# Kernel tuning notes

Hardware: AMD Instinct MI355X
Metric: run time of the kernel (lower is better)

The kernel has to match this reference:

```python
import jax, jax.numpy as jnp
import numpy as np

N_NODES = 100000
N_EDGES = 600000
D = 128
L = 4
BN_EPS = 1e-5


def setup_inputs() -> dict:
    key = jax.random.key(0)
    ks = jax.random.split(key, 12)
    x = jax.random.normal(ks[0], (N_NODES, D), dtype=jnp.float32)
    edge_index = jax.random.randint(ks[1], (2, N_EDGES), 0, N_NODES, dtype=jnp.int64)
    edge_attr = jax.random.uniform(ks[2], (N_EDGES, 1), dtype=jnp.float32)
    s = 0.05
    return {
        'x': x,
        'edge_index': edge_index,
        'edge_attr': edge_attr,
        'We': jax.random.normal(ks[3], (L, 1, D), dtype=jnp.float32) * s,   # GINE edge projection Linear(1, D)
        'be': jnp.zeros((L, D), dtype=jnp.float32),
        'eps': jnp.zeros((L,), dtype=jnp.float32),                          # train_eps=True, init 0
        'W1': jax.random.normal(ks[4], (L, D, D), dtype=jnp.float32) * s,
        'b1': jnp.zeros((L, D), dtype=jnp.float32),
        'gamma': jnp.ones((L, D), dtype=jnp.float32),
        'beta': jnp.zeros((L, D), dtype=jnp.float32),
        'W2': jax.random.normal(ks[5], (L, D, D), dtype=jnp.float32) * s,
        'b2': jnp.zeros((L, D), dtype=jnp.float32),
    }


def _gine_layer(h, src, dst, edge_attr, We, be, eps, W1, b1, gamma, beta, W2, b2):
    n = h.shape[0]
    e = edge_attr @ We + be                       # [E, D] edge embedding
    m = jax.nn.relu(h[src] + e)                   # gather + add + relu (messages)
    agg = jax.ops.segment_sum(m, dst, num_segments=n)  # scatter-add to destination nodes
    z = (1.0 + eps) * h + agg
    # MLP: Linear -> BatchNorm1d (training stats) -> ReLU -> Linear
    z = z @ W1 + b1
    mu = jnp.mean(z, axis=0)
    var = jnp.var(z, axis=0)                      # biased var, as in torch BN training
    z = (z - mu) * jax.lax.rsqrt(var + BN_EPS) * gamma + beta
    z = jax.nn.relu(z)
    return z @ W2 + b2


def reference(x, edge_index, edge_attr, We, be, eps, W1, b1, gamma, beta, W2, b2):
    src, dst = edge_index[0], edge_index[1]
    h = x
    for l in range(L):
        z = _gine_layer(h, src, dst, edge_attr, We[l], be[l], eps[l],
                        W1[l], b1[l], gamma[l], beta[l], W2[l], b2[l])
        r = jax.nn.relu(z)
        h = r if l == 0 else h + r
    return h
```

## Files before the change

kernel.cpp:

```cpp
#include <hip/hip_runtime.h>

#define NN 100000
#define NE 600000
#define DD 128
#define NL 4
#define GB 512
#define BKS 9
#define NBK ((NN + 511) >> 9)
#define CH 4096

typedef __attribute__((ext_vector_type(8))) short short8;
typedef __attribute__((ext_vector_type(4))) float float4v;
typedef __attribute__((ext_vector_type(2))) float f2;

__device__ inline unsigned short f2bf(float f) {
  union { float f; unsigned u; } v; v.f = f;
  unsigned r = v.u + 0x7fff + ((v.u >> 16) & 1);
  return (unsigned short)(r >> 16);
}
__device__ inline float bf2f(unsigned short u) {
  union { unsigned u; float f; } v; v.u = ((unsigned)u) << 16;
  return v.f;
}
__device__ inline f2 bfpair(unsigned u) {
  f2 r;
  r.x = __uint_as_float(u << 16);
  r.y = __uint_as_float(u & 0xffff0000u);
  return r;
}

__global__ void k_prep(const float* __restrict__ W1, const float* __restrict__ W2,
                       unsigned short* __restrict__ WT, int* __restrict__ counts,
                       float* __restrict__ stats4) {
  int i = blockIdx.x * 256 + threadIdx.x;
  if (i < NN) counts[i] = 0;
  if (i < NL * 256) stats4[i] = 0.f;
  if (i >= 8 * 16384) return;
  int m = i >> 14;
  int el = i & 16383;
  int k = el >> 7;
  int n = el & 127;
  const float* src = (m < 4) ? (W1 + (size_t)m * 16384) : (W2 + (size_t)(m - 4) * 16384);
  WT[(size_t)m * 16384 + n * 128 + k] = f2bf(src[k * 128 + n]);
}

__global__ void k_h2b(const float* __restrict__ src, unsigned short* __restrict__ dst,
                      const int* __restrict__ ei, int* __restrict__ counts) {
  int i = blockIdx.x * 256 + threadIdx.x;
  if (i < NE) atomicAdd(&counts[ei[NE + i]], 1);
  if (i >= NN * DD / 4) return;
  float4 v = ((const float4*)src)[i];
  ushort4 o;
  o.x = f2bf(v.x); o.y = f2bf(v.y); o.z = f2bf(v.z); o.w = f2bf(v.w);
  ((ushort4*)dst)[i] = o;
}

#define ST 256
#define SC 2
#define SB ((NN + ST * SC - 1) / (ST * SC))

__global__ void k_scan_part(const int* __restrict__ counts, int* __restrict__ row_ptr,
                            int* __restrict__ bsums) {
  __shared__ int s[ST];
  int b = blockIdx.x, t = threadIdx.x;
  int base = b * (ST * SC) + t * SC;
  int v0 = (base < NN) ? counts[base] : 0;
  int v1 = (base + 1 < NN) ? counts[base + 1] : 0;
  int tsum = v0 + v1;
  s[t] = tsum;
  __syncthreads();
  for (int d = 1; d < ST; d <<= 1) {
    int x = (t >= d) ? s[t - d] : 0;
    __syncthreads();
    s[t] += x;
    __syncthreads();
  }
  int excl = s[t] - tsum;
  if (base < NN) row_ptr[base] = excl;
  if (base + 1 < NN) row_ptr[base + 1] = excl + v0;
  if (t == ST - 1) bsums[b] = s[t];
}

__global__ void k_scan_bsum(const int* __restrict__ bsums, int* __restrict__ boffs,
                            int* __restrict__ row_ptr) {
  __shared__ int s[ST];
  int t = threadIdx.x;
  int v = (t < SB) ? bsums[t] : 0;
  s[t] = v;
  __syncthreads();
  for (int d = 1; d < ST; d <<= 1) {
    int x = (t >= d) ? s[t - d] : 0;
    __syncthreads();
    s[t] += x;
    __syncthreads();
  }
  if (t < SB) boffs[t] = s[t] - v;
  if (t == ST - 1) row_ptr[NN] = s[t];
}

__global__ void k_scan_add(const int* __restrict__ boffs, int* __restrict__ row_ptr,
                           int* __restrict__ scur) {
  int b = blockIdx.x, t = threadIdx.x;
  int base = b * (ST * SC) + t * SC;
  int o = boffs[b];
  if (base < NN) {
    int v = row_ptr[base] + o;
    row_ptr[base] = v;
    if ((base & 511) == 0) scur[base >> 9] = v;
  }
  if (base + 1 < NN) row_ptr[base + 1] += o;
}

__global__ __launch_bounds__(256) void k_bucket(
    const int* __restrict__ ei, const float* __restrict__ attr,
    int* __restrict__ scur, int2* __restrict__ staging) {
  __shared__ int cnt[256], cnt2[256], base[256], gbase[256], s[256];
  __shared__ int lpk[CH];
  __shared__ int lat[CH];
  __shared__ unsigned char lbk[CH];
  const int t = threadIdx.x;
  const int c0 = blockIdx.x * CH;
  const int n = min(CH, NE - c0);
  cnt[t] = 0;
  cnt2[t] = 0;
  __syncthreads();
  for (int k = t; k < n; k += 256) {
    int dst = ei[NE + c0 + k];
    atomicAdd(&cnt[dst >> BKS], 1);
  }
  __syncthreads();
  s[t] = cnt[t];
  __syncthreads();
  for (int d = 1; d < 256; d <<= 1) {
    int x = (t >= d) ? s[t - d] : 0;
    __syncthreads();
    s[t] += x;
    __syncthreads();
  }
  base[t] = s[t] - cnt[t];
  if (cnt[t] > 0) gbase[t] = atomicAdd(&scur[t], cnt[t]);
  __syncthreads();
  for (int k = t; k < n; k += 256) {
    int e = c0 + k;
    int src = ei[e];
    int dst = ei[NE + e];
    int b = dst >> BKS;
    int pos = base[b] + atomicAdd(&cnt2[b], 1);
    lpk[pos] = src | ((dst & 511) << 17);
    lat[pos] = __float_as_int(attr[e]);
    lbk[pos] = (unsigned char)b;
  }
  __syncthreads();
  for (int k = t; k < n; k += 256) {
    int b = lbk[k];
    staging[gbase[b] + (k - base[b])] = make_int2(lpk[k], lat[k]);
  }
}

__global__ __launch_bounds__(256) void k_place(
    const int* __restrict__ row_ptr, const int2* __restrict__ staging,
    int2* __restrict__ csr) {
  __shared__ int cur[512];
  const int b = blockIdx.x;
  const int n0 = b << BKS;
  const int nb = min(512, NN - n0);
  const int t = threadIdx.x;
  for (int j = t; j < nb; j += 256) cur[j] = row_ptr[n0 + j];
  __syncthreads();
  const int s0 = row_ptr[n0];
  const int s1 = row_ptr[n0 + nb];
  for (int i = s0 + t; i < s1; i += 256) {
    int2 r = staging[i];
    int j = ((unsigned)r.x) >> 17;
    int src = r.x & 0x1FFFF;
    int slot = atomicAdd(&cur[j], 1);
    csr[slot] = make_int2(src, r.y);
  }
}

#define CONS8(hv, at)                                                         \
  do {                                                                        \
    f2 av; av.x = (at); av.y = (at);                                          \
    f2 sx;                                                                    \
    sx = bfpair((hv).x) + (av * we01 + be01);                                 \
    a01 += __builtin_elementwise_max(sx, zero2);                              \
    sx = bfpair((hv).y) + (av * we23 + be23);                                 \
    a23 += __builtin_elementwise_max(sx, zero2);                              \
    sx = bfpair((hv).z) + (av * we45 + be45);                                 \
    a45 += __builtin_elementwise_max(sx, zero2);                              \
    sx = bfpair((hv).w) + (av * we67 + be67);                                 \
    a67 += __builtin_elementwise_max(sx, zero2);                              \
  } while (0)

#define LDROW(s) (*(const uint4*)(hb + (size_t)(s) * DD + d0))

__global__ __launch_bounds__(256) void k_agg(
    const unsigned short* __restrict__ hb,
    const int* __restrict__ row_ptr, const int2* __restrict__ csr,
    const float* __restrict__ We, const float* __restrict__ be,
    const float* __restrict__ epsp, unsigned short* __restrict__ zb) {
  const int tid0 = blockIdx.x * 256 + threadIdx.x;
  const int li = tid0 & 15;
  const int g0 = tid0 >> 4;
  const int NG = (gridDim.x * 256) >> 4;
  const int d0 = li * 8;

  const f2 we01 = *(const f2*)(We + d0);
  const f2 we23 = *(const f2*)(We + d0 + 2);
  const f2 we45 = *(const f2*)(We + d0 + 4);
  const f2 we67 = *(const f2*)(We + d0 + 6);
  const f2 be01 = *(const f2*)(be + d0);
  const f2 be23 = *(const f2*)(be + d0 + 2);
  const f2 be45 = *(const f2*)(be + d0 + 4);
  const f2 be67 = *(const f2*)(be + d0 + 6);
  const float ep = 1.f + epsp[0];
  f2 ep2; ep2.x = ep; ep2.y = ep;
  const f2 zero2 = {0.f, 0.f};

  for (int n = g0; n < NN; n += NG) {
    const int b = row_ptr[n], e = row_ptr[n + 1];
    const int deg = e - b;
    const int cnt = (deg < 16) ? deg : 16;
    int2 rec = (li < cnt) ? csr[b + li] : make_int2(0, 0);
    uint4 hs = LDROW(n);
    const int myidx = rec.x;
    const float myatt = __int_as_float(rec.y);
    f2 a01 = zero2, a23 = zero2, a45 = zero2, a67 = zero2;

    {
      int s0 = __shfl(myidx, 0, 16), s1 = __shfl(myidx, 1, 16);
      int s2 = __shfl(myidx, 2, 16), s3 = __shfl(myidx, 3, 16);
      int s4 = __shfl(myidx, 4, 16), s5 = __shfl(myidx, 5, 16);
      int s6 = __shfl(myidx, 6, 16), s7 = __shfl(myidx, 7, 16);
      float t0 = __shfl(myatt, 0, 16), t1 = __shfl(myatt, 1, 16);
      float t2 = __shfl(myatt, 2, 16), t3 = __shfl(myatt, 3, 16);
      float t4 = __shfl(myatt, 4, 16), t5 = __shfl(myatt, 5, 16);
      float t6 = __shfl(myatt, 6, 16), t7 = __shfl(myatt, 7, 16);
      uint4 h0 = LDROW(s0), h1 = LDROW(s1), h2 = LDROW(s2), h3 = LDROW(s3);
      uint4 h4 = LDROW(s4), h5 = LDROW(s5), h6 = LDROW(s6), h7 = LDROW(s7);
      if (cnt > 0) CONS8(h0, t0);
      if (cnt > 1) CONS8(h1, t1);
      if (cnt > 2) CONS8(h2, t2);
      if (cnt > 3) CONS8(h3, t3);
      if (cnt > 4) CONS8(h4, t4);
      if (cnt > 5) CONS8(h5, t5);
      if (cnt > 6) CONS8(h6, t6);
      if (cnt > 7) CONS8(h7, t7);
    }
    if (deg > 8) {
      int s0 = __shfl(myidx, 8, 16), s1 = __shfl(myidx, 9, 16);
      int s2 = __shfl(myidx, 10, 16), s3 = __shfl(myidx, 11, 16);
      int s4 = __shfl(myidx, 12, 16), s5 = __shfl(myidx, 13, 16);
      int s6 = __shfl(myidx, 14, 16), s7 = __shfl(myidx, 15, 16);
      float t0 = __shfl(myatt, 8, 16), t1 = __shfl(myatt, 9, 16);
      float t2 = __shfl(myatt, 10, 16), t3 = __shfl(myatt, 11, 16);
      float t4 = __shfl(myatt, 12, 16), t5 = __shfl(myatt, 13, 16);
      float t6 = __shfl(myatt, 14, 16), t7 = __shfl(myatt, 15, 16);
      uint4 h0 = LDROW(s0), h1 = LDROW(s1), h2 = LDROW(s2), h3 = LDROW(s3);
      uint4 h4 = LDROW(s4), h5 = LDROW(s5), h6 = LDROW(s6), h7 = LDROW(s7);
      if (cnt > 8)  CONS8(h0, t0);
      if (cnt > 9)  CONS8(h1, t1);
      if (cnt > 10) CONS8(h2, t2);
      if (cnt > 11) CONS8(h3, t3);
      if (cnt > 12) CONS8(h4, t4);
      if (cnt > 13) CONS8(h5, t5);
      if (cnt > 14) CONS8(h6, t6);
      if (cnt > 15) CONS8(h7, t7);
      for (int j = b + 16; j < e; j++) {
        int2 r2 = csr[j];
        float a = __int_as_float(r2.y);
        uint4 hv = LDROW(r2.x);
        CONS8(hv, a);
      }
    }

    f2 z01 = ep2 * bfpair(hs.x) + a01;
    f2 z23 = ep2 * bfpair(hs.y) + a23;
    f2 z45 = ep2 * bfpair(hs.z) + a45;
    f2 z67 = ep2 * bfpair(hs.w) + a67;
    uint4 o;
    o.x = (unsigned)f2bf(z01.x) | ((unsigned)f2bf(z01.y) << 16);
    o.y = (unsigned)f2bf(z23.x) | ((unsigned)f2bf(z23.y) << 16);
    o.z = (unsigned)f2bf(z45.x) | ((unsigned)f2bf(z45.y) << 16);
    o.w = (unsigned)f2bf(z67.x) | ((unsigned)f2bf(z67.y) << 16);
    *(uint4*)(zb + (size_t)n * DD + d0) = o;
  }
}

template <int MODE>
__global__ __launch_bounds__(512) void k_gemm(
    const unsigned short* __restrict__ Xb, const unsigned short* __restrict__ WT,
    const float* __restrict__ bias, float* __restrict__ stats,
    const float* __restrict__ gamma, const float* __restrict__ beta,
    const float* __restrict__ hprev, float* __restrict__ Yout,
    unsigned short* __restrict__ Ybf) {
  __shared__ unsigned short Wl[128 * 136];
  __shared__ unsigned short Xl[2][64 * 136];
  __shared__ float bns[256];
  const int tid = threadIdx.x;
  const int G = gridDim.x;
  const int NT = (NN + 63) >> 6;

  for (int i = tid; i < 2048; i += 512) {
    int rr = i >> 4, c = i & 15;
    *(uint4*)&Wl[rr * 136 + c * 8] = *(const uint4*)&WT[rr * 128 + c * 8];
  }

  const int lane = tid & 63;
  const int w = tid >> 6;
  const int m = lane & 15;
  const int quad = lane >> 4;
  const int rowblk = w & 3;
  const int ctbase = (w >> 2) * 4;

  float4 b4[4];
#pragma unroll
  for (int c = 0; c < 4; c++)
    b4[c] = *(const float4*)&bias[(ctbase + c) * 16 + quad * 4];

  const int c8 = tid & 15, rr16 = tid >> 4;
  float scl[8], sfl[8];
  if (MODE >= 1) {
    if (tid < 128) {
      const float invN = 1.f / (float)NN;
      float mu = stats[tid] * invN;
      float var = fmaxf(stats[128 + tid] * invN - mu * mu, 0.f);
      float xx = var + 1e-5f;
      float r = rsqrtf(xx);
      r = r * (1.5f - 0.5f * xx * r * r);
      float scale = gamma[tid] * r;
      bns[tid] = scale;
      bns[128 + tid] = beta[tid] - mu * scale;
    }
    __syncthreads();
#pragma unroll
    for (int j = 0; j < 8; j++) {
      scl[j] = bns[c8 * 8 + j];
      sfl[j] = bns[128 + c8 * 8 + j];
    }
  }

  uint4 xu[2];
  auto LOADR = [&](int t) {
    int r0 = t << 6;
#pragma unroll
    for (int it = 0; it < 2; it++) {
      int gr = r0 + rr16 + it * 32;
      xu[it] = (gr < NN) ? *(const uint4*)(Xb + (size_t)gr * DD + c8 * 8)
                         : make_uint4(0u, 0u, 0u, 0u);
    }
  };
  auto STORE_LDS = [&](int b) {
#pragma unroll
    for (int it = 0; it < 2; it++) {
      int row = rr16 + it * 32;
      uint4 u = xu[it];
      if (MODE >= 1) {
        unsigned p[4] = {u.x, u.y, u.z, u.w};
#pragma unroll
        for (int j = 0; j < 4; j++) {
          float lo = bf2f((unsigned short)(p[j] & 0xffffu));
          float hi = bf2f((unsigned short)(p[j] >> 16));
          lo = fmaxf(fmaf(lo, scl[2 * j], sfl[2 * j]), 0.f);
          hi = fmaxf(fmaf(hi, scl[2 * j + 1], sfl[2 * j + 1]), 0.f);
          p[j] = (unsigned)f2bf(lo) | ((unsigned)f2bf(hi) << 16);
        }
        u = make_uint4(p[0], p[1], p[2], p[3]);
      }
      *(uint4*)&Xl[b][row * 136 + c8 * 8] = u;
    }
  };

  float4v ssum[4], ssq[4];
  if (MODE == 0) {
#pragma unroll
    for (int c = 0; c < 4; c++) {
      ssum[c] = (float4v){0.f, 0.f, 0.f, 0.f};
      ssq[c] = (float4v){0.f, 0.f, 0.f, 0.f};
    }
  }

  const int t0 = blockIdx.x;
  LOADR(t0);
  STORE_LDS(0);
  if (t0 + G < NT) LOADR(t0 + G);
  __syncthreads();

  int buf = 0;
  for (int t = t0; t < NT; t += G) {
    const int nxt = t + G;
    if (nxt < NT) {
      STORE_LDS(buf ^ 1);
      if (nxt + G < NT) LOADR(nxt + G);
    }

    float4v acc[4];
#pragma unroll
    for (int c = 0; c < 4; c++)
      acc[c] = (float4v){b4[c].x, b4[c].y, b4[c].z, b4[c].w};

    const unsigned short* Ap = &Wl[(ctbase * 16 + m) * 136 + quad * 8];
    const unsigned short* Bp = &Xl[buf][(rowblk * 16 + m) * 136 + quad * 8];
#pragma unroll
    for (int q = 0; q < 4; q++) {
      short8 bfrag = *(const short8*)(Bp + q * 32);
#pragma unroll
      for (int c = 0; c < 4; c++) {
        short8 afrag = *(const short8*)(Ap + c * 16 * 136 + q * 32);
        acc[c] = __builtin_amdgcn_mfma_f32_16x16x32_bf16(afrag, bfrag, acc[c], 0, 0, 0);
      }
    }

    asm volatile("s_waitcnt lgkmcnt(0)" ::: "memory");
    __builtin_amdgcn_s_barrier();

    const int r = (t << 6) + rowblk * 16 + m;
    if (r < NN) {
      const size_t rb = (size_t)r * DD;
#pragma unroll
      for (int c = 0; c < 4; c++) {
        float4v v = acc[c];
        const int col = (ctbase + c) * 16 + quad * 4;
        if (MODE == 0) {
          ssum[c] += v;
          ssq[c] += v * v;
          ushort4 o;
          o.x = f2bf(v[0]); o.y = f2bf(v[1]); o.z = f2bf(v[2]); o.w = f2bf(v[3]);
          *(ushort4*)&Ybf[rb + col] = o;
        } else {
          v[0] = fmaxf(v[0], 0.f); v[1] = fmaxf(v[1], 0.f);
          v[2] = fmaxf(v[2], 0.f); v[3] = fmaxf(v[3], 0.f);
          if (MODE == 2) {
            float4 hp = *(const float4*)&hprev[rb + col];
            v[0] += hp.x; v[1] += hp.y; v[2] += hp.z; v[3] += hp.w;
          }
          *(float4v*)&Yout[rb + col] = v;
          if (Ybf) {
            ushort4 o;
            o.x = f2bf(v[0]); o.y = f2bf(v[1]); o.z = f2bf(v[2]); o.w = f2bf(v[3]);
            *(ushort4*)&Ybf[rb + col] = o;
          }
        }
      }
    }
    buf ^= 1;
  }

  if (MODE == 0) {
    float* sarr = (float*)Xl;
    float* sqarr = sarr + 512;
#pragma unroll
    for (int c = 0; c < 4; c++) {
      float4v s = ssum[c], s2 = ssq[c];
#pragma unroll
      for (int d = 1; d < 16; d <<= 1) {
#pragma unroll
        for (int j = 0; j < 4; j++) {
          s[j] += __shfl_xor(s[j], d);
          s2[j] += __shfl_xor(s2[j], d);
        }
      }
      if (m == 0) {
        *(float4v*)&sarr[w * 64 + c * 16 + quad * 4] = s;
        *(float4v*)&sqarr[w * 64 + c * 16 + quad * 4] = s2;
      }
    }
    __syncthreads();
    if (tid < 128) {
      const int ch = tid >> 6;
      const int cl = tid & 63;
      float s = 0.f, s2 = 0.f;
#pragma unroll
      for (int ww = 0; ww < 4; ww++) {
        s += sarr[(ch * 4 + ww) * 64 + cl];
        s2 += sqarr[(ch * 4 + ww) * 64 + cl];
      }
      atomicAdd(&stats[tid], s);
      atomicAdd(&stats[128 + tid], s2);
    }
  }
}

static inline size_t align256(size_t x) { return (x + 255) & ~(size_t)255; }

extern "C" void kernel_launch(void* const* d_in, const int* in_sizes, int n_in,
                              void* d_out, int out_size, void* d_ws, size_t ws_size,
                              hipStream_t stream) {
  const float* x     = (const float*)d_in[0];
  const int*   ei    = (const int*)d_in[1];
  const float* attr  = (const float*)d_in[2];
  const float* We    = (const float*)d_in[3];
  const float* be    = (const float*)d_in[4];
  const float* eps   = (const float*)d_in[5];
  const float* W1    = (const float*)d_in[6];
  const float* b1    = (const float*)d_in[7];
  const float* gamma = (const float*)d_in[8];
  const float* beta  = (const float*)d_in[9];
  const float* W2    = (const float*)d_in[10];
  const float* b2    = (const float*)d_in[11];
  float* out = (float*)d_out;

  char* w = (char*)d_ws;
  unsigned short* z2 = (unsigned short*)w; w += align256((size_t)NN * DD * 2);
  unsigned short* hb = (unsigned short*)w; w += align256((size_t)NN * DD * 2);
  unsigned short* zb = (unsigned short*)w; w += align256((size_t)NN * DD * 2);
  int*   row_ptr  = (int*)w;   w += align256((size_t)(NN + 1) * 4);
  int*   counts   = (int*)w;   w += align256((size_t)NN * 4);
  int*   scur     = (int*)w;   w += align256(256 * 4);
  int2*  csr      = (int2*)w;  w += align256((size_t)NE * 8);
  int2*  staging  = (int2*)w;  w += align256((size_t)NE * 8);
  float* stats4   = (float*)w; w += align256((size_t)NL * 256 * 4);
  int*   bsums    = (int*)w;   w += align256(ST * 4);
  int*   boffs    = (int*)w;   w += align256(ST * 4);
  unsigned short* WTb = (unsigned short*)w; w += align256((size_t)8 * 16384 * 2);

  k_prep<<<512, 256, 0, stream>>>(W1, W2, WTb, counts, stats4);
  k_h2b<<<(NN * DD / 4 + 255) / 256, 256, 0, stream>>>(x, hb, ei, counts);
  k_scan_part<<<SB, ST, 0, stream>>>(counts, row_ptr, bsums);
  k_scan_bsum<<<1, ST, 0, stream>>>(bsums, boffs, row_ptr);
  k_scan_add<<<SB, ST, 0, stream>>>(boffs, row_ptr, scur);
  k_bucket<<<(NE + CH - 1) / CH, 256, 0, stream>>>(ei, attr, scur, staging);
  k_place<<<NBK, 256, 0, stream>>>(row_ptr, staging, csr);

  for (int l = 0; l < NL; l++) {
    float* st = stats4 + (size_t)l * 256;
    k_agg<<<2048, 256, 0, stream>>>(
        hb, row_ptr, csr, We + l * DD, be + l * DD, eps + l, zb);
    k_gemm<0><<<GB, 512, 0, stream>>>(zb, WTb + (size_t)l * 16384, b1 + l * DD,
                                      st, nullptr, nullptr, nullptr, nullptr, z2);
    unsigned short* hbo = (l < NL - 1) ? hb : nullptr;
    if (l == 0)
      k_gemm<1><<<GB, 512, 0, stream>>>(z2, WTb + (size_t)(4 + l) * 16384, b2 + l * DD,
                                        st, gamma + l * DD, beta + l * DD,
                                        nullptr, out, hbo);
    else
      k_gemm<2><<<GB, 512, 0, stream>>>(z2, WTb + (size_t)(4 + l) * 16384, b2 + l * DD,
                                        st, gamma + l * DD, beta + l * DD,
                                        out, out, hbo);
  }
}
```

Before: 522.6 us.

## Prefetch all row tiles up front and unroll the GEMM tile loop

The dense GEMM/BN kernel now issues the global loads for all four of a block's row tiles before any compute, then processes the tiles in a fully unrolled sequence with LDS double-buffering. The residual hprev loads are hoisted ahead of the epilogue loop. The block-sum scan loop bound is also fixed to 256. This removes the loop-carried dependency on a single prefetch register set, so more memory latency is in flight at once. In exchange it uses more registers and hard-codes that each block handles at most four tiles; a smaller grid would skip rows.

```diff
diff --git a/kernel.cpp b/kernel.cpp
--- a/kernel.cpp
+++ b/kernel.cpp
@@ -88,7 +88,7 @@
   int v = (t < SB) ? bsums[t] : 0;
   s[t] = v;
   __syncthreads();
-  for (int d = 1; d < ST; d <<= 1) {
+  for (int d = 1; d < 256; d <<= 1) {
     int x = (t >= d) ? s[t - d] : 0;
     __syncthreads();
     s[t] += x;
@@ -340,21 +340,20 @@
     }
   }
 
-  uint4 xu[2];
-  auto LOADR = [&](int t) {
+  auto LOADR = [&](uint4 (&xr)[2], int t) {
     int r0 = t << 6;
 #pragma unroll
     for (int it = 0; it < 2; it++) {
       int gr = r0 + rr16 + it * 32;
-      xu[it] = (gr < NN) ? *(const uint4*)(Xb + (size_t)gr * DD + c8 * 8)
+      xr[it] = (gr < NN) ? *(const uint4*)(Xb + (size_t)gr * DD + c8 * 8)
                          : make_uint4(0u, 0u, 0u, 0u);
     }
   };
-  auto STORE_LDS = [&](int b) {
+  auto STORE_LDS = [&](uint4 (&xr)[2], int b) {
 #pragma unroll
     for (int it = 0; it < 2; it++) {
       int row = rr16 + it * 32;
-      uint4 u = xu[it];
+      uint4 u = xr[it];
       if (MODE >= 1) {
         unsigned p[4] = {u.x, u.y, u.z, u.w};
 #pragma unroll
@@ -380,27 +379,13 @@
     }
   }
 
-  const int t0 = blockIdx.x;
-  LOADR(t0);
-  STORE_LDS(0);
-  if (t0 + G < NT) LOADR(t0 + G);
-  __syncthreads();
-
-  int buf = 0;
-  for (int t = t0; t < NT; t += G) {
-    const int nxt = t + G;
-    if (nxt < NT) {
-      STORE_LDS(buf ^ 1);
-      if (nxt + G < NT) LOADR(nxt + G);
-    }
-
+  auto TILE = [&](int t, int bsel) {
     float4v acc[4];
 #pragma unroll
     for (int c = 0; c < 4; c++)
       acc[c] = (float4v){b4[c].x, b4[c].y, b4[c].z, b4[c].w};
-
     const unsigned short* Ap = &Wl[(ctbase * 16 + m) * 136 + quad * 8];
-    const unsigned short* Bp = &Xl[buf][(rowblk * 16 + m) * 136 + quad * 8];
+    const unsigned short* Bp = &Xl[bsel][(rowblk * 16 + m) * 136 + quad * 8];
 #pragma unroll
     for (int q = 0; q < 4; q++) {
       short8 bfrag = *(const short8*)(Bp + q * 32);
@@ -410,13 +395,18 @@
         acc[c] = __builtin_amdgcn_mfma_f32_16x16x32_bf16(afrag, bfrag, acc[c], 0, 0, 0);
       }
     }
-
     asm volatile("s_waitcnt lgkmcnt(0)" ::: "memory");
     __builtin_amdgcn_s_barrier();
 
     const int r = (t << 6) + rowblk * 16 + m;
     if (r < NN) {
       const size_t rb = (size_t)r * DD;
+      float4 hp[4];
+      if (MODE == 2) {
+#pragma unroll
+        for (int c = 0; c < 4; c++)
+          hp[c] = *(const float4*)&hprev[rb + (ctbase + c) * 16 + quad * 4];
+      }
 #pragma unroll
       for (int c = 0; c < 4; c++) {
         float4v v = acc[c];
@@ -431,8 +421,7 @@
           v[0] = fmaxf(v[0], 0.f); v[1] = fmaxf(v[1], 0.f);
           v[2] = fmaxf(v[2], 0.f); v[3] = fmaxf(v[3], 0.f);
           if (MODE == 2) {
-            float4 hp = *(const float4*)&hprev[rb + col];
-            v[0] += hp.x; v[1] += hp.y; v[2] += hp.z; v[3] += hp.w;
+            v[0] += hp[c].x; v[1] += hp[c].y; v[2] += hp[c].z; v[3] += hp[c].w;
           }
           *(float4v*)&Yout[rb + col] = v;
           if (Ybf) {
@@ -443,7 +432,28 @@
         }
       }
     }
-    buf ^= 1;
+  };
+
+  const int t0 = blockIdx.x;
+  const int t1 = t0 + G, t2 = t0 + 2 * G, t3 = t0 + 3 * G;
+  uint4 x0[2], x1[2], x2[2], x3[2];
+  LOADR(x0, t0);
+  if (t1 < NT) LOADR(x1, t1);
+  if (t2 < NT) LOADR(x2, t2);
+  if (t3 < NT) LOADR(x3, t3);
+  STORE_LDS(x0, 0);
+  __syncthreads();
+
+  if (t1 < NT) STORE_LDS(x1, 1);
+  TILE(t0, 0);
+  if (t1 < NT) {
+    if (t2 < NT) STORE_LDS(x2, 0);
+    TILE(t1, 1);
+    if (t2 < NT) {
+      if (t3 < NT) STORE_LDS(x3, 1);
+      TILE(t2, 0);
+      if (t3 < NT) TILE(t3, 1);
+    }
   }
 
   if (MODE == 0) {
```

Measured after the change: 514.4 us. About the same (-1.6%).
